# Optimization experiments

Measured on AMD Instinct MI355X. Metric: run time of the kernel, lower is better.

Reference implementation:

```python
import jax, jax.numpy as jnp
import numpy as np

B, H, S, D = 2, 16, 2048, 64
DEGREE = 2
EPS = 1e-4


def setup_inputs() -> dict:
    key = jax.random.key(0)
    kq, kk, kv = jax.random.split(key, 3)
    q = jax.random.normal(kq, (B, H, S, D), dtype=jnp.float32)
    k = jax.random.normal(kk, (B, H, S, D), dtype=jnp.float32)
    v = jax.random.normal(kv, (B, H, S, D), dtype=jnp.float32)
    return {"q": q, "k": k, "v": v}


def reference(q, k, v):
    # dots: [B,H,S,S] = QK^T
    dots = jnp.einsum("bhsd,bhtd->bhst", q, k)
    # polynomial kernel: x^degree, row-normalized with clamped denom
    x = dots ** DEGREE
    denom = jnp.maximum(x.sum(axis=-1, keepdims=True), EPS)
    attn = x / denom
    # weighted V sum: [B,H,S,D]
    return jnp.einsum("bhst,bhtd->bhsd", attn, v)
```

## Files before the change

kernel.cpp:

```cpp
#include <hip/hip_runtime.h>


#define S_LEN 2048
#define DH    64
#define BQ    128
#define BK    64
#define EPSTR 68
#define PSTR  65
#define BH_N  32
#define PER_BH (S_LEN * DH)
#define NT    (S_LEN / BK)

typedef __bf16 bf16x8 __attribute__((ext_vector_type(8)));
typedef __bf16 bf16x2 __attribute__((ext_vector_type(2)));
typedef float  f32x2  __attribute__((ext_vector_type(2)));
typedef float  f32x4  __attribute__((ext_vector_type(4)));
typedef float  f32x16 __attribute__((ext_vector_type(16)));
typedef unsigned int uivec2 __attribute__((ext_vector_type(2)));

__device__ __forceinline__ unsigned short f2bf(float f) {
    union { float f; unsigned int u; } x; x.f = f;
    unsigned int u = x.u;
    return (unsigned short)((u + 0x7fffu + ((u >> 16) & 1u)) >> 16);
}

__device__ __forceinline__ unsigned int pack2bf(float lo, float hi) {
#if __has_builtin(__builtin_amdgcn_cvt_pk_bf16_f32)
    bf16x2 p = __builtin_amdgcn_cvt_pk_bf16_f32(lo, hi);
    union { bf16x2 v; unsigned int u; } c; c.v = p;
    return c.u;
#else
    return (unsigned int)f2bf(lo) | ((unsigned int)f2bf(hi) << 16);
#endif
}

__device__ __forceinline__ void pl32swap(unsigned int& a, unsigned int& b) {
#if __has_builtin(__builtin_amdgcn_permlane32_swap)
    uivec2 r = __builtin_amdgcn_permlane32_swap(a, b, false, false);
    a = r[0]; b = r[1];
#else
    asm("v_permlane32_swap_b32 %0, %1" : "+v"(a), "+v"(b));
#endif
}

__global__ __launch_bounds__(256)
void prepass_kernel(const float* __restrict__ kg, const float* __restrict__ vg,
                    unsigned short* __restrict__ kfo, unsigned short* __restrict__ vfo)
{
    __shared__ unsigned short Lk[64 * 72];
    __shared__ unsigned short Lv[64 * PSTR];
    const int tid = threadIdx.x;
    const int bh  = blockIdx.y;
    const int t   = blockIdx.x;
    const size_t base = (size_t)bh * PER_BH + (size_t)t * 64 * DH;

    const float4* kf4 = (const float4*)(kg + base);
    const float4* vf4 = (const float4*)(vg + base);
    #pragma unroll
    for (int r = 0; r < 4; ++r) {
        int idx = r * 256 + tid;
        int row = idx >> 4, c4 = idx & 15;
        float4 f = kf4[idx];
        ushort4 hh;
        hh.x = f2bf(f.x); hh.y = f2bf(f.y); hh.z = f2bf(f.z); hh.w = f2bf(f.w);
        *(ushort4*)&Lk[row * 72 + c4 * 4] = hh;
        float4 g = vf4[idx];
        unsigned short* pv = &Lv[row * PSTR + c4 * 4];
        pv[0] = f2bf(g.x); pv[1] = f2bf(g.y); pv[2] = f2bf(g.z); pv[3] = f2bf(g.w);
    }
    __syncthreads();

    unsigned short* kout = kfo + (size_t)bh * PER_BH + (size_t)t * 4096;
    #pragma unroll
    for (int r = 0; r < 2; ++r) {
        int pos = r * 256 + tid;
        int lam = pos & 63, rest = pos >> 6;
        int e = rest >> 2, ks = rest & 3;
        int l31 = lam & 31, h = lam >> 5;
        uint4 v = *(const uint4*)&Lk[(e * 32 + l31) * 72 + ks * 16 + h * 8];
        *(uint4*)(kout + (size_t)pos * 8) = v;
    }
    unsigned short* vout = vfo + (size_t)bh * PER_BH + (size_t)t * 4096;
    #pragma unroll
    for (int r = 0; r < 2; ++r) {
        int pos = r * 256 + tid;
        int lam = pos & 63, rest = pos >> 6;
        int e = rest >> 2, ksl = (rest >> 1) & 1, mt = rest & 1;
        int l31 = lam & 31, h = lam >> 5;
        int d  = mt * 32 + l31;
        int j0 = e * 32 + ksl * 16 + h * 8;
        union { unsigned short s[8]; uint4 u; } u;
        #pragma unroll
        for (int jj = 0; jj < 8; ++jj) u.s[jj] = Lv[(j0 + jj) * PSTR + d];
        *(uint4*)(vout + (size_t)pos * 8) = u.u;
    }
}

__global__ __launch_bounds__(256, 2)
void poly_attn_main(const float* __restrict__ qg,
                    const unsigned short* __restrict__ kfo,
                    const unsigned short* __restrict__ vfo,
                    float* __restrict__ og)
{
    __shared__ float epb[8 * 32 * EPSTR];
    __shared__ float dbuf[256];

    const int tid  = threadIdx.x;
    const int lane = tid & 63;
    const int w    = tid >> 6;
    const int p    = w >> 1;
    const int e    = w & 1;
    const int l31  = lane & 31;
    const int h    = lane >> 5;

    const int id = blockIdx.x;
    const int r5 = id & 31;
    const int bh = (r5 & 7) * 4 + (r5 >> 3);
    const int qt = id >> 5;
    const int q0 = qt * BQ;

    const float* qb = qg + ((size_t)bh * S_LEN + q0) * DH;
    const unsigned short* kw = kfo + (size_t)bh * PER_BH + e * 2048 + (size_t)lane * 8;
    const unsigned short* vw = vfo + (size_t)bh * PER_BH + e * 2048 + (size_t)lane * 8;
    float* ob = og + ((size_t)bh * S_LEN + q0) * DH;

    bf16x8 qfrag[2][4];
    #pragma unroll
    for (int s = 0; s < 2; ++s) {
        #pragma unroll
        for (int ks = 0; ks < 4; ++ks) {
            const float* qp = qb + (64 * p + 32 * s + l31) * DH + ks * 16 + h * 8;
            float4 f0 = *(const float4*)qp;
            float4 f1 = *(const float4*)(qp + 4);
            union { unsigned int d[4]; bf16x8 v; } u;
            u.d[0] = pack2bf(f0.x, f0.y);
            u.d[1] = pack2bf(f0.z, f0.w);
            u.d[2] = pack2bf(f1.x, f1.y);
            u.d[3] = pack2bf(f1.z, f1.w);
            qfrag[s][ks] = u.v;
        }
    }

    f32x16 oacc[2][2];
    #pragma unroll
    for (int s = 0; s < 2; ++s)
        #pragma unroll
        for (int mt = 0; mt < 2; ++mt)
            #pragma unroll
            for (int r = 0; r < 16; ++r) oacc[s][mt][r] = 0.f;
    f32x2 ds2[2];
    ds2[0][0]=0.f; ds2[0][1]=0.f; ds2[1][0]=0.f; ds2[1][1]=0.f;

    uint4 kbuf[2][4], vbuf[2][4];
    unsigned int bsave[2][2][4];

    #pragma unroll
    for (int x = 0; x < 4; ++x) {
        kbuf[0][x] = *(const uint4*)(kw + x * 512);
        vbuf[0][x] = *(const uint4*)(vw + x * 512);
        kbuf[1][x] = *(const uint4*)(kw + 4096 + x * 512);
    }

#define QK_STAGE(KI)                                                                \
        f32x16 acc0, acc1;                                                          \
        _Pragma("unroll")                                                           \
        for (int r = 0; r < 16; ++r) { acc0[r] = 0.f; acc1[r] = 0.f; }              \
        _Pragma("unroll")                                                           \
        for (int ks = 0; ks < 4; ++ks) {                                            \
            union { uint4 u; bf16x8 v; } kc; kc.u = kbuf[KI][ks];                   \
            acc0 = __builtin_amdgcn_mfma_f32_32x32x16_bf16(kc.v, qfrag[0][ks], acc0, 0, 0, 0); \
            acc1 = __builtin_amdgcn_mfma_f32_32x32x16_bf16(kc.v, qfrag[1][ks], acc1, 0, 0, 0); \
        }

#define PV_STAGE(VI)                                                                \
        _Pragma("unroll")                                                           \
        for (int s = 0; s < 2; ++s) {                                               \
            _Pragma("unroll")                                                       \
            for (int ksl = 0; ksl < 2; ++ksl) {                                     \
                union { unsigned int d[4]; bf16x8 v; } bu;                          \
                bu.d[0] = bsave[s][ksl][0]; bu.d[1] = bsave[s][ksl][1];             \
                bu.d[2] = bsave[s][ksl][2]; bu.d[3] = bsave[s][ksl][3];             \
                _Pragma("unroll")                                                   \
                for (int mt = 0; mt < 2; ++mt) {                                    \
                    union { uint4 u; bf16x8 v; } vv; vv.u = vbuf[VI][ksl * 2 + mt]; \
                    oacc[s][mt] = __builtin_amdgcn_mfma_f32_32x32x16_bf16(vv.v, bu.v, oacc[s][mt], 0, 0, 0); \
                }                                                                   \
            }                                                                       \
        }

#define XF_STAGE()                                                                  \
        _Pragma("unroll")                                                           \
        for (int s = 0; s < 2; ++s) {                                               \
            unsigned int pk[4][2];                                                  \
            _Pragma("unroll")                                                       \
            for (int g = 0; g < 4; ++g) {                                           \
                f32x2 v01, v23;                                                     \
                v01[0] = (s ? acc1 : acc0)[4*g+0]; v01[1] = (s ? acc1 : acc0)[4*g+1]; \
                v23[0] = (s ? acc1 : acc0)[4*g+2]; v23[1] = (s ? acc1 : acc0)[4*g+3]; \
                v01 = v01 * v01; v23 = v23 * v23;                                   \
                ds2[s] += v01; ds2[s] += v23;                                       \
                pk[g][0] = pack2bf(v01[0], v01[1]);                                 \
                pk[g][1] = pack2bf(v23[0], v23[1]);                                 \
            }                                                                       \
            _Pragma("unroll")                                                       \
            for (int ksl = 0; ksl < 2; ++ksl) {                                     \
                unsigned int a0 = pk[2*ksl][0], b0 = pk[2*ksl+1][0];                \
                unsigned int a1 = pk[2*ksl][1], b1 = pk[2*ksl+1][1];                \
                pl32swap(a0, b0);                                                   \
                pl32swap(a1, b1);                                                   \
                bsave[s][ksl][0] = a0; bsave[s][ksl][1] = a1;                       \
                bsave[s][ksl][2] = b0; bsave[s][ksl][3] = b1;                       \
            }                                                                       \
        }

    { QK_STAGE(0); XF_STAGE(); }

#define BODY(T, KC, KN, VL, VC, DO_KPF)                                             \
    {                                                                               \
        if (DO_KPF) {                                                               \
            const unsigned short* kn_ = kw + (size_t)((T) + 1) * 4096;              \
            _Pragma("unroll")                                                       \
            for (int x = 0; x < 4; ++x) kbuf[KN][x] = *(const uint4*)(kn_ + x * 512); \
        }                                                                           \
        {                                                                           \
            const unsigned short* vn_ = vw + (size_t)(T) * 4096;                    \
            _Pragma("unroll")                                                       \
            for (int x = 0; x < 4; ++x) vbuf[VL][x] = *(const uint4*)(vn_ + x * 512); \
        }                                                                           \
        QK_STAGE(KC);                                                               \
        PV_STAGE(VC);                                                               \
        XF_STAGE();                                                                 \
    }

    for (int tp = 1; tp < NT - 1; tp += 2) {
        BODY(tp,     1, 0, 1, 0, true);
        BODY(tp + 1, 0, 1, 0, 1, true);
    }
    BODY(NT - 1, 1, 0, 1, 0, false);
    { PV_STAGE(1); }
#undef BODY
#undef QK_STAGE
#undef PV_STAGE
#undef XF_STAGE

    float wavetot[2];
    #pragma unroll
    for (int s = 0; s < 2; ++s) {
        float t = ds2[s][0] + ds2[s][1];
        wavetot[s] = t + __shfl_xor(t, 32);
    }

    #pragma unroll
    for (int s = 0; s < 2; ++s) {
        float* ep = epb + (size_t)(w * 2 + s) * (32 * EPSTR);
        #pragma unroll
        for (int mt = 0; mt < 2; ++mt) {
            #pragma unroll
            for (int g = 0; g < 4; ++g) {
                f32x4 vv;
                vv[0] = oacc[s][mt][4*g+0];
                vv[1] = oacc[s][mt][4*g+1];
                vv[2] = oacc[s][mt][4*g+2];
                vv[3] = oacc[s][mt][4*g+3];
                *(f32x4*)&ep[l31 * EPSTR + mt * 32 + 8 * g + 4 * h] = vv;
            }
        }
        if (h == 0) dbuf[(w * 2 + s) * 32 + l31] = wavetot[s];
    }
    __syncthreads();

    const int psrc = w >> 1, ssrc = w & 1;
    const int r0 = (2 * psrc + 0) * 2 + ssrc;
    const int r1 = (2 * psrc + 1) * 2 + ssrc;
    const int lr = lane >> 1;
    const float den = dbuf[r0 * 32 + lr] + dbuf[r1 * 32 + lr];
    const float inv = 1.0f / fmaxf(den, 1e-4f);
    const float* ea = epb + (size_t)r0 * (32 * EPSTR) + lr * EPSTR;
    const float* eb = epb + (size_t)r1 * (32 * EPSTR) + lr * EPSTR;
    #pragma unroll
    for (int it = 0; it < 8; ++it) {
        int d0 = (lane & 1) * 32 + it * 4;
        f32x4 a = *(const f32x4*)&ea[d0];
        f32x4 b = *(const f32x4*)&eb[d0];
        f32x4 sm;
        sm[0] = (a[0] + b[0]) * inv;
        sm[1] = (a[1] + b[1]) * inv;
        sm[2] = (a[2] + b[2]) * inv;
        sm[3] = (a[3] + b[3]) * inv;
        *(f32x4*)&ob[(32 * w + lr) * DH + d0] = sm;
    }
}

#define LSTR 72
__global__ __launch_bounds__(256, 2)
void poly_attn_fallback(const float* __restrict__ qg, const float* __restrict__ kg,
                        const float* __restrict__ vg, float* __restrict__ og)
{
    __shared__ unsigned short Qs[64 * LSTR];
    __shared__ unsigned short Ksl[64 * LSTR];
    __shared__ unsigned short Vt[64 * LSTR];
    __shared__ unsigned short Xsl[64 * LSTR];

    const int tid  = threadIdx.x;
    const int lane = tid & 63;
    const int w    = tid >> 6;
    const int c    = lane & 15;
    const int quad = lane >> 4;
    const int i0   = w * 16;

    const int bh = blockIdx.y;
    const int q0 = blockIdx.x * 64;

    const float* qb = qg + ((size_t)bh * S_LEN + q0) * DH;
    const float* kb = kg + (size_t)bh * S_LEN * DH;
    const float* vb = vg + (size_t)bh * S_LEN * DH;
    float*       ob = og + ((size_t)bh * S_LEN + q0) * DH;

    {
        const float4* qf4 = (const float4*)qb;
        #pragma unroll
        for (int r = 0; r < 4; ++r) {
            int idx = r * 256 + tid;
            int row = idx >> 4, c4 = idx & 15;
            float4 f = qf4[idx];
            ushort4 hh;
            hh.x = f2bf(f.x); hh.y = f2bf(f.y); hh.z = f2bf(f.z); hh.w = f2bf(f.w);
            *(ushort4*)&Qs[row * LSTR + c4 * 4] = hh;
        }
    }

    f32x4 oacc[4];
    #pragma unroll
    for (int t = 0; t < 4; ++t) { oacc[t][0]=0.f; oacc[t][1]=0.f; oacc[t][2]=0.f; oacc[t][3]=0.f; }
    float dsum[4] = {0.f, 0.f, 0.f, 0.f};

    for (int t0 = 0; t0 < S_LEN; t0 += 64) {
        __syncthreads();
        {
            const float4* kf4 = (const float4*)(kb + (size_t)t0 * DH);
            const float4* vf4 = (const float4*)(vb + (size_t)t0 * DH);
            #pragma unroll
            for (int r = 0; r < 4; ++r) {
                int idx = r * 256 + tid;
                int row = idx >> 4, c4 = idx & 15;
                float4 f = kf4[idx];
                ushort4 hh;
                hh.x = f2bf(f.x); hh.y = f2bf(f.y); hh.z = f2bf(f.z); hh.w = f2bf(f.w);
                *(ushort4*)&Ksl[row * LSTR + c4 * 4] = hh;
                float4 g = vf4[idx];
                int d0 = c4 * 4;
                Vt[(d0 + 0) * LSTR + row] = f2bf(g.x);
                Vt[(d0 + 1) * LSTR + row] = f2bf(g.y);
                Vt[(d0 + 2) * LSTR + row] = f2bf(g.z);
                Vt[(d0 + 3) * LSTR + row] = f2bf(g.w);
            }
        }
        __syncthreads();

        f32x4 xacc[4];
        #pragma unroll
        for (int t = 0; t < 4; ++t) { xacc[t][0]=0.f; xacc[t][1]=0.f; xacc[t][2]=0.f; xacc[t][3]=0.f; }
        #pragma unroll
        for (int k0 = 0; k0 < 64; k0 += 32) {
            bf16x8 af = *(const bf16x8*)&Qs[(i0 + c) * LSTR + k0 + quad * 8];
            #pragma unroll
            for (int tn = 0; tn < 4; ++tn) {
                bf16x8 bfg = *(const bf16x8*)&Ksl[(tn * 16 + c) * LSTR + k0 + quad * 8];
                xacc[tn] = __builtin_amdgcn_mfma_f32_16x16x32_bf16(af, bfg, xacc[tn], 0, 0, 0);
            }
        }
        #pragma unroll
        for (int tn = 0; tn < 4; ++tn)
            #pragma unroll
            for (int r = 0; r < 4; ++r) {
                float xv = xacc[tn][r];
                float xs = xv * xv;
                dsum[r] += xs;
                Xsl[(i0 + quad * 4 + r) * LSTR + tn * 16 + c] = f2bf(xs);
            }
        __syncthreads();

        #pragma unroll
        for (int k0 = 0; k0 < 64; k0 += 32) {
            bf16x8 af = *(const bf16x8*)&Xsl[(i0 + c) * LSTR + k0 + quad * 8];
            #pragma unroll
            for (int tn = 0; tn < 4; ++tn) {
                bf16x8 bfg = *(const bf16x8*)&Vt[(tn * 16 + c) * LSTR + k0 + quad * 8];
                oacc[tn] = __builtin_amdgcn_mfma_f32_16x16x32_bf16(af, bfg, oacc[tn], 0, 0, 0);
            }
        }
    }

    #pragma unroll
    for (int r = 0; r < 4; ++r) {
        float s = dsum[r];
        s += __shfl_xor(s, 1);
        s += __shfl_xor(s, 2);
        s += __shfl_xor(s, 4);
        s += __shfl_xor(s, 8);
        dsum[r] = 1.0f / fmaxf(s, 1e-4f);
    }
    #pragma unroll
    for (int tn = 0; tn < 4; ++tn)
        #pragma unroll
        for (int r = 0; r < 4; ++r)
            ob[(i0 + quad * 4 + r) * DH + tn * 16 + c] = oacc[tn][r] * dsum[r];
}

extern "C" void kernel_launch(void* const* d_in, const int* in_sizes, int n_in,
                              void* d_out, int out_size, void* d_ws, size_t ws_size,
                              hipStream_t stream) {
    (void)in_sizes; (void)n_in; (void)out_size;
    const float* q = (const float*)d_in[0];
    const float* k = (const float*)d_in[1];
    const float* v = (const float*)d_in[2];
    float* o = (float*)d_out;

    const size_t elems = (size_t)BH_N * PER_BH;
    const size_t need  = 2 * elems * sizeof(unsigned short);

    if (ws_size >= need) {
        unsigned short* kfo = (unsigned short*)d_ws;
        unsigned short* vfo = kfo + elems;
        prepass_kernel<<<dim3(NT, BH_N), 256, 0, stream>>>(k, v, kfo, vfo);
        poly_attn_main<<<dim3(BH_N * S_LEN / BQ), 256, 0, stream>>>(q, kfo, vfo, o);
    } else {
        poly_attn_fallback<<<dim3(S_LEN / 64, BH_N), 256, 0, stream>>>(q, k, v, o);
    }
}
```

Baseline: 133.2 us.

## Halve query tile per block and single-buffer K/V to raise occupancy

Shrinks the query tile from 128 to 64 rows, so each wave handles one 32-row query slice instead of two. The K/V register double-buffers become single buffers with pointer-advancing loads, and launch bounds rise to 4 blocks per CU. The smaller footprint is meant to allow more resident waves to hide latency. In exchange, K/V tiles are reloaded twice as often across blocks, each loaded K/V fragment feeds half as many MFMAs, and there is less prefetch depth inside each wave.

```diff
diff --git a/kernel.cpp b/kernel.cpp
--- a/kernel.cpp
+++ b/kernel.cpp
@@ -3,7 +3,7 @@
 
 #define S_LEN 2048
 #define DH    64
-#define BQ    128
+#define BQ    64
 #define BK    64
 #define EPSTR 68
 #define PSTR  65
@@ -96,19 +96,19 @@
     }
 }
 
-__global__ __launch_bounds__(256, 2)
+__global__ __launch_bounds__(256, 4)
 void poly_attn_main(const float* __restrict__ qg,
                     const unsigned short* __restrict__ kfo,
                     const unsigned short* __restrict__ vfo,
                     float* __restrict__ og)
 {
-    __shared__ float epb[8 * 32 * EPSTR];
-    __shared__ float dbuf[256];
+    __shared__ float epb[4 * 32 * EPSTR];
+    __shared__ float dbuf[128];
 
     const int tid  = threadIdx.x;
     const int lane = tid & 63;
     const int w    = tid >> 6;
-    const int p    = w >> 1;
+    const int sp   = w >> 1;
     const int e    = w & 1;
     const int l31  = lane & 31;
     const int h    = lane >> 5;
@@ -124,162 +124,136 @@
     const unsigned short* vw = vfo + (size_t)bh * PER_BH + e * 2048 + (size_t)lane * 8;
     float* ob = og + ((size_t)bh * S_LEN + q0) * DH;
 
-    bf16x8 qfrag[2][4];
-    #pragma unroll
-    for (int s = 0; s < 2; ++s) {
-        #pragma unroll
-        for (int ks = 0; ks < 4; ++ks) {
-            const float* qp = qb + (64 * p + 32 * s + l31) * DH + ks * 16 + h * 8;
-            float4 f0 = *(const float4*)qp;
-            float4 f1 = *(const float4*)(qp + 4);
-            union { unsigned int d[4]; bf16x8 v; } u;
-            u.d[0] = pack2bf(f0.x, f0.y);
-            u.d[1] = pack2bf(f0.z, f0.w);
-            u.d[2] = pack2bf(f1.x, f1.y);
-            u.d[3] = pack2bf(f1.z, f1.w);
-            qfrag[s][ks] = u.v;
-        }
-    }
-
-    f32x16 oacc[2][2];
-    #pragma unroll
-    for (int s = 0; s < 2; ++s)
-        #pragma unroll
-        for (int mt = 0; mt < 2; ++mt)
-            #pragma unroll
-            for (int r = 0; r < 16; ++r) oacc[s][mt][r] = 0.f;
-    f32x2 ds2[2];
-    ds2[0][0]=0.f; ds2[0][1]=0.f; ds2[1][0]=0.f; ds2[1][1]=0.f;
-
-    uint4 kbuf[2][4], vbuf[2][4];
-    unsigned int bsave[2][2][4];
-
-    #pragma unroll
-    for (int x = 0; x < 4; ++x) {
-        kbuf[0][x] = *(const uint4*)(kw + x * 512);
-        vbuf[0][x] = *(const uint4*)(vw + x * 512);
-        kbuf[1][x] = *(const uint4*)(kw + 4096 + x * 512);
-    }
-
-#define QK_STAGE(KI)                                                                \
-        f32x16 acc0, acc1;                                                          \
+    bf16x8 qfrag[4];
+    #pragma unroll
+    for (int ks = 0; ks < 4; ++ks) {
+        const float* qp = qb + (32 * sp + l31) * DH + ks * 16 + h * 8;
+        float4 f0 = *(const float4*)qp;
+        float4 f1 = *(const float4*)(qp + 4);
+        union { unsigned int d[4]; bf16x8 v; } u;
+        u.d[0] = pack2bf(f0.x, f0.y);
+        u.d[1] = pack2bf(f0.z, f0.w);
+        u.d[2] = pack2bf(f1.x, f1.y);
+        u.d[3] = pack2bf(f1.z, f1.w);
+        qfrag[ks] = u.v;
+    }
+
+    f32x16 oacc[2];
+    #pragma unroll
+    for (int mt = 0; mt < 2; ++mt)
+        #pragma unroll
+        for (int r = 0; r < 16; ++r) oacc[mt][r] = 0.f;
+    f32x2 ds2; ds2[0] = 0.f; ds2[1] = 0.f;
+
+    uint4 kbuf[4], vbuf[4];
+    unsigned int bsave[2][4];
+
+    const unsigned short* kload = kw;
+    const unsigned short* vload = vw;
+    #pragma unroll
+    for (int x = 0; x < 4; ++x) kbuf[x] = *(const uint4*)(kload + x * 512);
+    kload += 4096;
+
+#define KLOAD()                                                                     \
+        { _Pragma("unroll")                                                         \
+          for (int x = 0; x < 4; ++x) kbuf[x] = *(const uint4*)(kload + x * 512);   \
+          kload += 4096; }
+
+#define VLOAD()                                                                     \
+        { _Pragma("unroll")                                                         \
+          for (int x = 0; x < 4; ++x) vbuf[x] = *(const uint4*)(vload + x * 512);   \
+          vload += 4096; }
+
+#define QK_STAGE()                                                                  \
+        f32x16 acc;                                                                 \
         _Pragma("unroll")                                                           \
-        for (int r = 0; r < 16; ++r) { acc0[r] = 0.f; acc1[r] = 0.f; }              \
+        for (int r = 0; r < 16; ++r) acc[r] = 0.f;                                  \
         _Pragma("unroll")                                                           \
         for (int ks = 0; ks < 4; ++ks) {                                            \
-            union { uint4 u; bf16x8 v; } kc; kc.u = kbuf[KI][ks];                   \
-            acc0 = __builtin_amdgcn_mfma_f32_32x32x16_bf16(kc.v, qfrag[0][ks], acc0, 0, 0, 0); \
-            acc1 = __builtin_amdgcn_mfma_f32_32x32x16_bf16(kc.v, qfrag[1][ks], acc1, 0, 0, 0); \
-        }
-
-#define PV_STAGE(VI)                                                                \
+            union { uint4 u; bf16x8 v; } kc; kc.u = kbuf[ks];                       \
+            acc = __builtin_amdgcn_mfma_f32_32x32x16_bf16(kc.v, qfrag[ks], acc, 0, 0, 0); \
+        }
+
+#define PV_STAGE()                                                                  \
         _Pragma("unroll")                                                           \
-        for (int s = 0; s < 2; ++s) {                                               \
+        for (int ksl = 0; ksl < 2; ++ksl) {                                         \
+            union { unsigned int d[4]; bf16x8 v; } bu;                              \
+            bu.d[0] = bsave[ksl][0]; bu.d[1] = bsave[ksl][1];                       \
+            bu.d[2] = bsave[ksl][2]; bu.d[3] = bsave[ksl][3];                       \
             _Pragma("unroll")                                                       \
-            for (int ksl = 0; ksl < 2; ++ksl) {                                     \
-                union { unsigned int d[4]; bf16x8 v; } bu;                          \
-                bu.d[0] = bsave[s][ksl][0]; bu.d[1] = bsave[s][ksl][1];             \
-                bu.d[2] = bsave[s][ksl][2]; bu.d[3] = bsave[s][ksl][3];             \
-                _Pragma("unroll")                                                   \
-                for (int mt = 0; mt < 2; ++mt) {                                    \
-                    union { uint4 u; bf16x8 v; } vv; vv.u = vbuf[VI][ksl * 2 + mt]; \
-                    oacc[s][mt] = __builtin_amdgcn_mfma_f32_32x32x16_bf16(vv.v, bu.v, oacc[s][mt], 0, 0, 0); \
-                }                                                                   \
+            for (int mt = 0; mt < 2; ++mt) {                                        \
+                union { uint4 u; bf16x8 v; } vv; vv.u = vbuf[ksl * 2 + mt];         \
+                oacc[mt] = __builtin_amdgcn_mfma_f32_32x32x16_bf16(vv.v, bu.v, oacc[mt], 0, 0, 0); \
             }                                                                       \
         }
 
 #define XF_STAGE()                                                                  \
         _Pragma("unroll")                                                           \
-        for (int s = 0; s < 2; ++s) {                                               \
-            unsigned int pk[4][2];                                                  \
-            _Pragma("unroll")                                                       \
-            for (int g = 0; g < 4; ++g) {                                           \
-                f32x2 v01, v23;                                                     \
-                v01[0] = (s ? acc1 : acc0)[4*g+0]; v01[1] = (s ? acc1 : acc0)[4*g+1]; \
-                v23[0] = (s ? acc1 : acc0)[4*g+2]; v23[1] = (s ? acc1 : acc0)[4*g+3]; \
-                v01 = v01 * v01; v23 = v23 * v23;                                   \
-                ds2[s] += v01; ds2[s] += v23;                                       \
-                pk[g][0] = pack2bf(v01[0], v01[1]);                                 \
-                pk[g][1] = pack2bf(v23[0], v23[1]);                                 \
-            }                                                                       \
-            _Pragma("unroll")                                                       \
-            for (int ksl = 0; ksl < 2; ++ksl) {                                     \
-                unsigned int a0 = pk[2*ksl][0], b0 = pk[2*ksl+1][0];                \
-                unsigned int a1 = pk[2*ksl][1], b1 = pk[2*ksl+1][1];                \
-                pl32swap(a0, b0);                                                   \
-                pl32swap(a1, b1);                                                   \
-                bsave[s][ksl][0] = a0; bsave[s][ksl][1] = a1;                       \
-                bsave[s][ksl][2] = b0; bsave[s][ksl][3] = b1;                       \
-            }                                                                       \
-        }
-
-    { QK_STAGE(0); XF_STAGE(); }
-
-#define BODY(T, KC, KN, VL, VC, DO_KPF)                                             \
-    {                                                                               \
-        if (DO_KPF) {                                                               \
-            const unsigned short* kn_ = kw + (size_t)((T) + 1) * 4096;              \
-            _Pragma("unroll")                                                       \
-            for (int x = 0; x < 4; ++x) kbuf[KN][x] = *(const uint4*)(kn_ + x * 512); \
-        }                                                                           \
-        {                                                                           \
-            const unsigned short* vn_ = vw + (size_t)(T) * 4096;                    \
-            _Pragma("unroll")                                                       \
-            for (int x = 0; x < 4; ++x) vbuf[VL][x] = *(const uint4*)(vn_ + x * 512); \
-        }                                                                           \
-        QK_STAGE(KC);                                                               \
-        PV_STAGE(VC);                                                               \
-        XF_STAGE();                                                                 \
-    }
-
-    for (int tp = 1; tp < NT - 1; tp += 2) {
-        BODY(tp,     1, 0, 1, 0, true);
-        BODY(tp + 1, 0, 1, 0, 1, true);
-    }
-    BODY(NT - 1, 1, 0, 1, 0, false);
-    { PV_STAGE(1); }
-#undef BODY
+        for (int ksl = 0; ksl < 2; ++ksl) {                                         \
+            f32x2 va, vb, vc, vd;                                                   \
+            va[0] = acc[8*ksl+0]; va[1] = acc[8*ksl+1];                             \
+            vb[0] = acc[8*ksl+2]; vb[1] = acc[8*ksl+3];                             \
+            vc[0] = acc[8*ksl+4]; vc[1] = acc[8*ksl+5];                             \
+            vd[0] = acc[8*ksl+6]; vd[1] = acc[8*ksl+7];                             \
+            va = va * va; vb = vb * vb; vc = vc * vc; vd = vd * vd;                 \
+            ds2 += va; ds2 += vb; ds2 += vc; ds2 += vd;                             \
+            unsigned int a0 = pack2bf(va[0], va[1]);                                \
+            unsigned int a1 = pack2bf(vb[0], vb[1]);                                \
+            unsigned int b0 = pack2bf(vc[0], vc[1]);                                \
+            unsigned int b1 = pack2bf(vd[0], vd[1]);                                \
+            pl32swap(a0, b0);                                                       \
+            pl32swap(a1, b1);                                                       \
+            bsave[ksl][0] = a0; bsave[ksl][1] = a1;                                 \
+            bsave[ksl][2] = b0; bsave[ksl][3] = b1;                                 \
+        }
+
+    { QK_STAGE(); KLOAD(); XF_STAGE(); }
+
+    for (int T = 1; T < NT - 1; ++T) {
+        VLOAD();
+        QK_STAGE();
+        KLOAD();
+        PV_STAGE();
+        XF_STAGE();
+    }
+    { VLOAD(); QK_STAGE(); PV_STAGE(); XF_STAGE(); }
+    { VLOAD(); PV_STAGE(); }
+#undef KLOAD
+#undef VLOAD
 #undef QK_STAGE
 #undef PV_STAGE
 #undef XF_STAGE
 
-    float wavetot[2];
-    #pragma unroll
-    for (int s = 0; s < 2; ++s) {
-        float t = ds2[s][0] + ds2[s][1];
-        wavetot[s] = t + __shfl_xor(t, 32);
-    }
-
-    #pragma unroll
-    for (int s = 0; s < 2; ++s) {
-        float* ep = epb + (size_t)(w * 2 + s) * (32 * EPSTR);
+    float wavetot;
+    { float t = ds2[0] + ds2[1]; wavetot = t + __shfl_xor(t, 32); }
+
+    {
+        float* ep = epb + (size_t)w * (32 * EPSTR);
         #pragma unroll
         for (int mt = 0; mt < 2; ++mt) {
             #pragma unroll
             for (int g = 0; g < 4; ++g) {
                 f32x4 vv;
-                vv[0] = oacc[s][mt][4*g+0];
-                vv[1] = oacc[s][mt][4*g+1];
-                vv[2] = oacc[s][mt][4*g+2];
-                vv[3] = oacc[s][mt][4*g+3];
+                vv[0] = oacc[mt][4*g+0];
+                vv[1] = oacc[mt][4*g+1];
+                vv[2] = oacc[mt][4*g+2];
+                vv[3] = oacc[mt][4*g+3];
                 *(f32x4*)&ep[l31 * EPSTR + mt * 32 + 8 * g + 4 * h] = vv;
             }
         }
-        if (h == 0) dbuf[(w * 2 + s) * 32 + l31] = wavetot[s];
+        if (h == 0) dbuf[w * 32 + l31] = wavetot;
     }
     __syncthreads();
 
-    const int psrc = w >> 1, ssrc = w & 1;
-    const int r0 = (2 * psrc + 0) * 2 + ssrc;
-    const int r1 = (2 * psrc + 1) * 2 + ssrc;
+    const int so = w >> 1, ho = w & 1;
     const int lr = lane >> 1;
-    const float den = dbuf[r0 * 32 + lr] + dbuf[r1 * 32 + lr];
+    const float den = dbuf[(2 * so + 0) * 32 + lr] + dbuf[(2 * so + 1) * 32 + lr];
     const float inv = 1.0f / fmaxf(den, 1e-4f);
-    const float* ea = epb + (size_t)r0 * (32 * EPSTR) + lr * EPSTR;
-    const float* eb = epb + (size_t)r1 * (32 * EPSTR) + lr * EPSTR;
-    #pragma unroll
-    for (int it = 0; it < 8; ++it) {
-        int d0 = (lane & 1) * 32 + it * 4;
+    const float* ea = epb + (size_t)(2 * so + 0) * (32 * EPSTR) + lr * EPSTR;
+    const float* eb = epb + (size_t)(2 * so + 1) * (32 * EPSTR) + lr * EPSTR;
+    #pragma unroll
+    for (int it = 0; it < 4; ++it) {
+        int d0 = ho * 32 + (lane & 1) * 16 + it * 4;
         f32x4 a = *(const f32x4*)&ea[d0];
         f32x4 b = *(const f32x4*)&eb[d0];
         f32x4 sm;
@@ -287,7 +261,7 @@
         sm[1] = (a[1] + b[1]) * inv;
         sm[2] = (a[2] + b[2]) * inv;
         sm[3] = (a[3] + b[3]) * inv;
-        *(f32x4*)&ob[(32 * w + lr) * DH + d0] = sm;
+        *(f32x4*)&ob[(32 * so + lr) * DH + d0] = sm;
     }
 }
 
```

Result: slower. 139.8 us (+4.9%).

## Stage K/V tiles through LDS with async global_load_lds four-slot ring

Applied to the files above, without the earlier changes.

Replaces per-wave register prefetch of K/V fragments with a cooperative four-deep LDS ring filled by global_load_lds DMA. Waves 0-1 load K and waves 2-3 load V, each tile is shared across waves, and vmcnt waits plus barriers gate consumption. It also adds setprio around the MFMA blocks and drops the software-pipelined QK/PV interleave. The aim is to hide global latency and free registers, at the cost of two barriers per tile and a larger LDS footprint, which may lower occupancy.

```diff
diff --git a/kernel.cpp b/kernel.cpp
--- a/kernel.cpp
+++ b/kernel.cpp
@@ -10,6 +10,8 @@
 #define BH_N  32
 #define PER_BH (S_LEN * DH)
 #define NT    (S_LEN / BK)
+#define SLOT_BYTES 16384
+#define SMEM_BYTES 70656
 
 typedef __bf16 bf16x8 __attribute__((ext_vector_type(8)));
 typedef __bf16 bf16x2 __attribute__((ext_vector_type(2)));
@@ -41,6 +43,12 @@
 #else
     asm("v_permlane32_swap_b32 %0, %1" : "+v"(a), "+v"(b));
 #endif
+}
+
+__device__ __forceinline__ void dma16(const void* g, void* l) {
+    __builtin_amdgcn_global_load_lds(
+        (const __attribute__((address_space(1))) unsigned int*)g,
+        (__attribute__((address_space(3))) unsigned int*)l, 16, 0, 0);
 }
 
 __global__ __launch_bounds__(256)
@@ -102,8 +110,7 @@
                     const unsigned short* __restrict__ vfo,
                     float* __restrict__ og)
 {
-    __shared__ float epb[8 * 32 * EPSTR];
-    __shared__ float dbuf[256];
+    __shared__ __align__(16) unsigned char smem[SMEM_BYTES];
 
     const int tid  = threadIdx.x;
     const int lane = tid & 63;
@@ -120,8 +127,6 @@
     const int q0 = qt * BQ;
 
     const float* qb = qg + ((size_t)bh * S_LEN + q0) * DH;
-    const unsigned short* kw = kfo + (size_t)bh * PER_BH + e * 2048 + (size_t)lane * 8;
-    const unsigned short* vw = vfo + (size_t)bh * PER_BH + e * 2048 + (size_t)lane * 8;
     float* ob = og + ((size_t)bh * S_LEN + q0) * DH;
 
     bf16x8 qfrag[2][4];
@@ -140,6 +145,23 @@
             qfrag[s][ks] = u.v;
         }
     }
+    __builtin_amdgcn_sched_barrier(0);
+
+    const unsigned short* gw =
+        ((w < 2) ? kfo : vfo) + (size_t)bh * PER_BH + (w & 1) * 2048 + (size_t)lane * 8;
+    const int ldsoff = ((w < 2) ? 0 : 8192) + (w & 1) * 4096;
+
+#define DMA_TILE(TT)                                                                \
+    {                                                                               \
+        const unsigned short* gs_ = gw + (size_t)(TT) * 4096;                       \
+        unsigned char* lb_ = smem + ((TT) & 3) * SLOT_BYTES + ldsoff;               \
+        dma16(gs_,        lb_);                                                     \
+        dma16(gs_ + 512,  lb_ + 1024);                                              \
+        dma16(gs_ + 1024, lb_ + 2048);                                              \
+        dma16(gs_ + 1536, lb_ + 3072);                                              \
+    }
+
+    DMA_TILE(0) DMA_TILE(1) DMA_TILE(2) DMA_TILE(3)
 
     f32x16 oacc[2][2];
     #pragma unroll
@@ -151,44 +173,51 @@
     f32x2 ds2[2];
     ds2[0][0]=0.f; ds2[0][1]=0.f; ds2[1][0]=0.f; ds2[1][1]=0.f;
 
-    uint4 kbuf[2][4], vbuf[2][4];
-    unsigned int bsave[2][2][4];
-
-    #pragma unroll
-    for (int x = 0; x < 4; ++x) {
-        kbuf[0][x] = *(const uint4*)(kw + x * 512);
-        vbuf[0][x] = *(const uint4*)(vw + x * 512);
-        kbuf[1][x] = *(const uint4*)(kw + 4096 + x * 512);
-    }
-
-#define QK_STAGE(KI)                                                                \
+    f32x16 zacc;
+    #pragma unroll
+    for (int r = 0; r < 16; ++r) zacc[r] = 0.f;
+    asm volatile("" : "+v"(zacc));
+
+    unsigned int bsv[2][2][4];
+
+#define WAITVM_(N) asm volatile("s_waitcnt vmcnt(" #N ")" ::: "memory")
+#define WAITVM(N) WAITVM_(N)
+
+#define STEP(TT, VM, ISSUE)                                                         \
+    {                                                                               \
+        WAITVM(VM);                                                                 \
+        __builtin_amdgcn_s_barrier();                                               \
+        asm volatile("" ::: "memory");                                              \
+        __builtin_amdgcn_sched_barrier(0);                                          \
+        const unsigned char* sb_ = smem + ((TT) & 3) * SLOT_BYTES;                  \
+        const unsigned char* kp_ = sb_ + e * 4096 + (size_t)lane * 16;              \
+        const unsigned char* vp_ = sb_ + 8192 + e * 4096 + (size_t)lane * 16;       \
+        uint4 kf0 = *(const uint4*)(kp_);                                           \
+        uint4 kf1 = *(const uint4*)(kp_ + 1024);                                    \
+        uint4 kf2 = *(const uint4*)(kp_ + 2048);                                    \
+        uint4 kf3 = *(const uint4*)(kp_ + 3072);                                    \
+        uint4 vf0 = *(const uint4*)(vp_);                                           \
+        uint4 vf1 = *(const uint4*)(vp_ + 1024);                                    \
+        uint4 vf2 = *(const uint4*)(vp_ + 2048);                                    \
+        uint4 vf3 = *(const uint4*)(vp_ + 3072);                                    \
         f32x16 acc0, acc1;                                                          \
-        _Pragma("unroll")                                                           \
-        for (int r = 0; r < 16; ++r) { acc0[r] = 0.f; acc1[r] = 0.f; }              \
-        _Pragma("unroll")                                                           \
-        for (int ks = 0; ks < 4; ++ks) {                                            \
-            union { uint4 u; bf16x8 v; } kc; kc.u = kbuf[KI][ks];                   \
-            acc0 = __builtin_amdgcn_mfma_f32_32x32x16_bf16(kc.v, qfrag[0][ks], acc0, 0, 0, 0); \
-            acc1 = __builtin_amdgcn_mfma_f32_32x32x16_bf16(kc.v, qfrag[1][ks], acc1, 0, 0, 0); \
-        }
-
-#define PV_STAGE(VI)                                                                \
-        _Pragma("unroll")                                                           \
-        for (int s = 0; s < 2; ++s) {                                               \
-            _Pragma("unroll")                                                       \
-            for (int ksl = 0; ksl < 2; ++ksl) {                                     \
-                union { unsigned int d[4]; bf16x8 v; } bu;                          \
-                bu.d[0] = bsave[s][ksl][0]; bu.d[1] = bsave[s][ksl][1];             \
-                bu.d[2] = bsave[s][ksl][2]; bu.d[3] = bsave[s][ksl][3];             \
-                _Pragma("unroll")                                                   \
-                for (int mt = 0; mt < 2; ++mt) {                                    \
-                    union { uint4 u; bf16x8 v; } vv; vv.u = vbuf[VI][ksl * 2 + mt]; \
-                    oacc[s][mt] = __builtin_amdgcn_mfma_f32_32x32x16_bf16(vv.v, bu.v, oacc[s][mt], 0, 0, 0); \
-                }                                                                   \
-            }                                                                       \
-        }
-
-#define XF_STAGE()                                                                  \
+        __builtin_amdgcn_s_setprio(1);                                              \
+        {                                                                           \
+            union { uint4 u; bf16x8 v; } kc;                                        \
+            kc.u = kf0;                                                             \
+            acc0 = __builtin_amdgcn_mfma_f32_32x32x16_bf16(kc.v, qfrag[0][0], zacc, 0, 0, 0); \
+            acc1 = __builtin_amdgcn_mfma_f32_32x32x16_bf16(kc.v, qfrag[1][0], zacc, 0, 0, 0); \
+            kc.u = kf1;                                                             \
+            acc0 = __builtin_amdgcn_mfma_f32_32x32x16_bf16(kc.v, qfrag[0][1], acc0, 0, 0, 0); \
+            acc1 = __builtin_amdgcn_mfma_f32_32x32x16_bf16(kc.v, qfrag[1][1], acc1, 0, 0, 0); \
+            kc.u = kf2;                                                             \
+            acc0 = __builtin_amdgcn_mfma_f32_32x32x16_bf16(kc.v, qfrag[0][2], acc0, 0, 0, 0); \
+            acc1 = __builtin_amdgcn_mfma_f32_32x32x16_bf16(kc.v, qfrag[1][2], acc1, 0, 0, 0); \
+            kc.u = kf3;                                                             \
+            acc0 = __builtin_amdgcn_mfma_f32_32x32x16_bf16(kc.v, qfrag[0][3], acc0, 0, 0, 0); \
+            acc1 = __builtin_amdgcn_mfma_f32_32x32x16_bf16(kc.v, qfrag[1][3], acc1, 0, 0, 0); \
+        }                                                                           \
+        __builtin_amdgcn_s_setprio(0);                                              \
         _Pragma("unroll")                                                           \
         for (int s = 0; s < 2; ++s) {                                               \
             unsigned int pk[4][2];                                                  \
@@ -208,40 +237,42 @@
                 unsigned int a1 = pk[2*ksl][1], b1 = pk[2*ksl+1][1];                \
                 pl32swap(a0, b0);                                                   \
                 pl32swap(a1, b1);                                                   \
-                bsave[s][ksl][0] = a0; bsave[s][ksl][1] = a1;                       \
-                bsave[s][ksl][2] = b0; bsave[s][ksl][3] = b1;                       \
+                bsv[s][ksl][0] = a0; bsv[s][ksl][1] = a1;                           \
+                bsv[s][ksl][2] = b0; bsv[s][ksl][3] = b1;                           \
             }                                                                       \
-        }
-
-    { QK_STAGE(0); XF_STAGE(); }
-
-#define BODY(T, KC, KN, VL, VC, DO_KPF)                                             \
-    {                                                                               \
-        if (DO_KPF) {                                                               \
-            const unsigned short* kn_ = kw + (size_t)((T) + 1) * 4096;              \
+        }                                                                           \
+        __builtin_amdgcn_s_setprio(1);                                              \
+        _Pragma("unroll")                                                           \
+        for (int s = 0; s < 2; ++s) {                                               \
             _Pragma("unroll")                                                       \
-            for (int x = 0; x < 4; ++x) kbuf[KN][x] = *(const uint4*)(kn_ + x * 512); \
+            for (int ksl = 0; ksl < 2; ++ksl) {                                     \
+                union { unsigned int d[4]; bf16x8 v; } bu;                          \
+                bu.d[0] = bsv[s][ksl][0]; bu.d[1] = bsv[s][ksl][1];                 \
+                bu.d[2] = bsv[s][ksl][2]; bu.d[3] = bsv[s][ksl][3];                 \
+                union { uint4 u; bf16x8 v; } vv;                                    \
+                vv.u = (ksl == 0 ? vf0 : vf2);                                      \
+                oacc[s][0] = __builtin_amdgcn_mfma_f32_32x32x16_bf16(vv.v, bu.v, oacc[s][0], 0, 0, 0); \
+                vv.u = (ksl == 0 ? vf1 : vf3);                                      \
+                oacc[s][1] = __builtin_amdgcn_mfma_f32_32x32x16_bf16(vv.v, bu.v, oacc[s][1], 0, 0, 0); \
+            }                                                                       \
         }                                                                           \
-        {                                                                           \
-            const unsigned short* vn_ = vw + (size_t)(T) * 4096;                    \
-            _Pragma("unroll")                                                       \
-            for (int x = 0; x < 4; ++x) vbuf[VL][x] = *(const uint4*)(vn_ + x * 512); \
-        }                                                                           \
-        QK_STAGE(KC);                                                               \
-        PV_STAGE(VC);                                                               \
-        XF_STAGE();                                                                 \
-    }
-
-    for (int tp = 1; tp < NT - 1; tp += 2) {
-        BODY(tp,     1, 0, 1, 0, true);
-        BODY(tp + 1, 0, 1, 0, 1, true);
-    }
-    BODY(NT - 1, 1, 0, 1, 0, false);
-    { PV_STAGE(1); }
-#undef BODY
-#undef QK_STAGE
-#undef PV_STAGE
-#undef XF_STAGE
+        __builtin_amdgcn_s_setprio(0);                                              \
+        __builtin_amdgcn_s_barrier();                                               \
+        asm volatile("" ::: "memory");                                              \
+        if (ISSUE) DMA_TILE((TT) + 4)                                               \
+    }
+
+    for (int T = 0; T < NT - 4; ++T) {
+        STEP(T, 12, 1);
+    }
+    STEP(NT - 4, 12, 0);
+    STEP(NT - 3,  8, 0);
+    STEP(NT - 2,  4, 0);
+    STEP(NT - 1,  0, 0);
+#undef STEP
+#undef DMA_TILE
+#undef WAITVM
+#undef WAITVM_
 
     float wavetot[2];
     #pragma unroll
@@ -250,6 +281,8 @@
         wavetot[s] = t + __shfl_xor(t, 32);
     }
 
+    float* epb  = (float*)smem;
+    float* dbuf = (float*)(smem + 69632);
     #pragma unroll
     for (int s = 0; s < 2; ++s) {
         float* ep = epb + (size_t)(w * 2 + s) * (32 * EPSTR);
```

Result: slower. 137.2 us (+3.0%).

## Stagger per-wave KV tile order and deepen K prefetch in polynomial attention

Applied to the files above, without the earlier changes.

Each wave now starts its walk over the 32 K/V tiles at a different offset (w*8, wrapping mod 32), so waves in a block read different tiles at the same moment instead of all hitting the same addresses. The K prefetch is reissued after the QK MFMAs to load two tiles ahead. The QK accumulator init is taken from a pinned zero vector rather than zeroing registers each step. Row sums and the output are order-independent, so results stay the same, but the extra K prefetch distance and wrap-around indexing add register pressure and may wrap past the last tile with a redundant load.

```diff
diff --git a/kernel.cpp b/kernel.cpp
--- a/kernel.cpp
+++ b/kernel.cpp
@@ -124,6 +124,11 @@
     const unsigned short* vw = vfo + (size_t)bh * PER_BH + e * 2048 + (size_t)lane * 8;
     float* ob = og + ((size_t)bh * S_LEN + q0) * DH;
 
+    const int off = w * 8;
+
+#define KPTR(t) (kw + (size_t)(((t) + off) & 31) * 4096)
+#define VPTR(t) (vw + (size_t)(((t) + off) & 31) * 4096)
+
     bf16x8 qfrag[2][4];
     #pragma unroll
     for (int s = 0; s < 2; ++s) {
@@ -151,40 +156,54 @@
     f32x2 ds2[2];
     ds2[0][0]=0.f; ds2[0][1]=0.f; ds2[1][0]=0.f; ds2[1][1]=0.f;
 
+    f32x16 zacc;
+    #pragma unroll
+    for (int r = 0; r < 16; ++r) zacc[r] = 0.f;
+    asm volatile("" : "+v"(zacc));
+
     uint4 kbuf[2][4], vbuf[2][4];
-    unsigned int bsave[2][2][4];
-
-    #pragma unroll
-    for (int x = 0; x < 4; ++x) {
-        kbuf[0][x] = *(const uint4*)(kw + x * 512);
-        vbuf[0][x] = *(const uint4*)(vw + x * 512);
-        kbuf[1][x] = *(const uint4*)(kw + 4096 + x * 512);
-    }
-
-#define QK_STAGE(KI)                                                                \
+    unsigned int bsv[2][2][4];
+
+#define LOADK(BI, T)                                                                \
+    { const unsigned short* kp_ = KPTR(T);                                          \
+      _Pragma("unroll")                                                             \
+      for (int x = 0; x < 4; ++x) kbuf[BI][x] = *(const uint4*)(kp_ + x * 512); }
+#define LOADV(BI, T)                                                                \
+    { const unsigned short* vp_ = VPTR(T);                                          \
+      _Pragma("unroll")                                                             \
+      for (int x = 0; x < 4; ++x) vbuf[BI][x] = *(const uint4*)(vp_ + x * 512); }
+
+#define QK_STAGE(KC)                                                                \
         f32x16 acc0, acc1;                                                          \
-        _Pragma("unroll")                                                           \
-        for (int r = 0; r < 16; ++r) { acc0[r] = 0.f; acc1[r] = 0.f; }              \
-        _Pragma("unroll")                                                           \
-        for (int ks = 0; ks < 4; ++ks) {                                            \
-            union { uint4 u; bf16x8 v; } kc; kc.u = kbuf[KI][ks];                   \
-            acc0 = __builtin_amdgcn_mfma_f32_32x32x16_bf16(kc.v, qfrag[0][ks], acc0, 0, 0, 0); \
-            acc1 = __builtin_amdgcn_mfma_f32_32x32x16_bf16(kc.v, qfrag[1][ks], acc1, 0, 0, 0); \
-        }
-
-#define PV_STAGE(VI)                                                                \
+        {                                                                           \
+            union { uint4 u; bf16x8 v; } kc;                                        \
+            kc.u = kbuf[KC][0];                                                     \
+            acc0 = __builtin_amdgcn_mfma_f32_32x32x16_bf16(kc.v, qfrag[0][0], zacc, 0, 0, 0); \
+            acc1 = __builtin_amdgcn_mfma_f32_32x32x16_bf16(kc.v, qfrag[1][0], zacc, 0, 0, 0); \
+            kc.u = kbuf[KC][1];                                                     \
+            acc0 = __builtin_amdgcn_mfma_f32_32x32x16_bf16(kc.v, qfrag[0][1], acc0, 0, 0, 0); \
+            acc1 = __builtin_amdgcn_mfma_f32_32x32x16_bf16(kc.v, qfrag[1][1], acc1, 0, 0, 0); \
+            kc.u = kbuf[KC][2];                                                     \
+            acc0 = __builtin_amdgcn_mfma_f32_32x32x16_bf16(kc.v, qfrag[0][2], acc0, 0, 0, 0); \
+            acc1 = __builtin_amdgcn_mfma_f32_32x32x16_bf16(kc.v, qfrag[1][2], acc1, 0, 0, 0); \
+            kc.u = kbuf[KC][3];                                                     \
+            acc0 = __builtin_amdgcn_mfma_f32_32x32x16_bf16(kc.v, qfrag[0][3], acc0, 0, 0, 0); \
+            acc1 = __builtin_amdgcn_mfma_f32_32x32x16_bf16(kc.v, qfrag[1][3], acc1, 0, 0, 0); \
+        }
+
+#define PV_STAGE(VC)                                                                \
         _Pragma("unroll")                                                           \
         for (int s = 0; s < 2; ++s) {                                               \
             _Pragma("unroll")                                                       \
             for (int ksl = 0; ksl < 2; ++ksl) {                                     \
                 union { unsigned int d[4]; bf16x8 v; } bu;                          \
-                bu.d[0] = bsave[s][ksl][0]; bu.d[1] = bsave[s][ksl][1];             \
-                bu.d[2] = bsave[s][ksl][2]; bu.d[3] = bsave[s][ksl][3];             \
-                _Pragma("unroll")                                                   \
-                for (int mt = 0; mt < 2; ++mt) {                                    \
-                    union { uint4 u; bf16x8 v; } vv; vv.u = vbuf[VI][ksl * 2 + mt]; \
-                    oacc[s][mt] = __builtin_amdgcn_mfma_f32_32x32x16_bf16(vv.v, bu.v, oacc[s][mt], 0, 0, 0); \
-                }                                                                   \
+                bu.d[0] = bsv[s][ksl][0]; bu.d[1] = bsv[s][ksl][1];                 \
+                bu.d[2] = bsv[s][ksl][2]; bu.d[3] = bsv[s][ksl][3];                 \
+                union { uint4 u; bf16x8 v; } vv;                                    \
+                vv.u = vbuf[VC][ksl * 2 + 0];                                       \
+                oacc[s][0] = __builtin_amdgcn_mfma_f32_32x32x16_bf16(vv.v, bu.v, oacc[s][0], 0, 0, 0); \
+                vv.u = vbuf[VC][ksl * 2 + 1];                                       \
+                oacc[s][1] = __builtin_amdgcn_mfma_f32_32x32x16_bf16(vv.v, bu.v, oacc[s][1], 0, 0, 0); \
             }                                                                       \
         }
 
@@ -208,40 +227,37 @@
                 unsigned int a1 = pk[2*ksl][1], b1 = pk[2*ksl+1][1];                \
                 pl32swap(a0, b0);                                                   \
                 pl32swap(a1, b1);                                                   \
-                bsave[s][ksl][0] = a0; bsave[s][ksl][1] = a1;                       \
-                bsave[s][ksl][2] = b0; bsave[s][ksl][3] = b1;                       \
+                bsv[s][ksl][0] = a0; bsv[s][ksl][1] = a1;                           \
+                bsv[s][ksl][2] = b0; bsv[s][ksl][3] = b1;                           \
             }                                                                       \
         }
 
-    { QK_STAGE(0); XF_STAGE(); }
-
-#define BODY(T, KC, KN, VL, VC, DO_KPF)                                             \
+    LOADK(0, 0) LOADK(1, 1) LOADV(0, 0)
+    { QK_STAGE(0); LOADK(0, 2); XF_STAGE(); }
+
+#define BODY(TT, KC, VL, VC)                                                        \
     {                                                                               \
-        if (DO_KPF) {                                                               \
-            const unsigned short* kn_ = kw + (size_t)((T) + 1) * 4096;              \
-            _Pragma("unroll")                                                       \
-            for (int x = 0; x < 4; ++x) kbuf[KN][x] = *(const uint4*)(kn_ + x * 512); \
-        }                                                                           \
-        {                                                                           \
-            const unsigned short* vn_ = vw + (size_t)(T) * 4096;                    \
-            _Pragma("unroll")                                                       \
-            for (int x = 0; x < 4; ++x) vbuf[VL][x] = *(const uint4*)(vn_ + x * 512); \
-        }                                                                           \
+        LOADV(VL, TT)                                                               \
         QK_STAGE(KC);                                                               \
+        LOADK(KC, (TT) + 2)                                                         \
         PV_STAGE(VC);                                                               \
         XF_STAGE();                                                                 \
     }
 
-    for (int tp = 1; tp < NT - 1; tp += 2) {
-        BODY(tp,     1, 0, 1, 0, true);
-        BODY(tp + 1, 0, 1, 0, 1, true);
-    }
-    BODY(NT - 1, 1, 0, 1, 0, false);
+    for (int T = 1; T + 1 < NT; T += 2) {
+        BODY(T,     1, 1, 0);
+        BODY(T + 1, 0, 0, 1);
+    }
+    BODY(NT - 1, 1, 1, 0);
     { PV_STAGE(1); }
 #undef BODY
 #undef QK_STAGE
 #undef PV_STAGE
 #undef XF_STAGE
+#undef LOADK
+#undef LOADV
+#undef KPTR
+#undef VPTR
 
     float wavetot[2];
     #pragma unroll
```

After: 137.8 us. 3.4% more time.
